# Kernel optimization log

Hardware: AMD Instinct MI355X
Metric: run time of the kernel (lower is better)

## Reference

```python
import jax, jax.numpy as jnp
import numpy as np

N_RES = 30000
N_ATOMS = 6
N_EDGES = 300000
HIDDEN = 128
N_GRAPHS = 32
CENTRAL_IDX = 1
EPS = 1e-6


def _normalize(x, axis=-1):
    # matches torch F.normalize (eps=1e-12 on the norm)
    return x / jnp.maximum(jnp.linalg.norm(x, axis=axis, keepdims=True), 1e-12)


def _rbf(D, D_min=0.0, D_max=20.0, num_rbf=16):
    mu = jnp.linspace(D_min, D_max, num_rbf)
    sigma = (D_max - D_min) / num_rbf
    return jnp.exp(-(((D[..., None] - mu) / sigma) ** 2))


def _quaternions(R):
    Rxx, Ryy, Rzz = R[:, 0, 0], R[:, 1, 1], R[:, 2, 2]
    mag = 0.5 * jnp.sqrt(jnp.abs(1.0 + jnp.stack([Rxx - Ryy - Rzz, -Rxx + Ryy - Rzz, -Rxx - Ryy + Rzz], -1)))
    signs = jnp.sign(jnp.stack([R[:, 2, 1] - R[:, 1, 2], R[:, 0, 2] - R[:, 2, 0], R[:, 1, 0] - R[:, 0, 1]], -1))
    xyz = signs * mag
    w = jnp.sqrt(jax.nn.relu(1.0 + Rxx + Ryy + Rzz))[:, None] / 2.0
    return _normalize(jnp.concatenate([xyz, w], -1))


def _layernorm(x, w, b, eps=1e-5):
    mu = x.mean(-1, keepdims=True)
    var = ((x - mu) ** 2).mean(-1, keepdims=True)
    return (x - mu) / jnp.sqrt(var + eps) * w + b


def _forward(coords, central_coords, node_W, node_b, node_ln_w, node_ln_b,
             edge_W, edge_b, edge_ln_w, edge_ln_b, batch, edge_index):
    n_res, n_atoms = coords.shape[:2]
    L = n_res * n_atoms
    src, tgt = edge_index[0], edge_index[1]

    # chain-boundary masks (replace torch's NaN-write + nan_to_num with masking to 0)
    boundary = jnp.concatenate([jnp.zeros(1, bool), batch[1:] != batch[:-1]])      # first res of new graph
    boundary_next = jnp.concatenate([boundary[1:], jnp.zeros(1, bool)])            # last res of a graph

    Xf = coords.reshape(-1, 3)
    ar = jnp.arange(L)
    col = jnp.arange(n_atoms)

    # ---- dihedral ----
    U = _normalize(Xf[1:] - Xf[:-1])
    c1 = _normalize(jnp.cross(U[:-2], U[1:-1]))
    c2 = _normalize(jnp.cross(U[1:-1], U[2:]))
    dih = jnp.arccos(jnp.clip((c1 * c2).sum(-1), -1.0 + EPS, 1.0 - EPS)) * jnp.sign((c2 * U[:-2]).sum(-1))
    dih = jnp.pad(dih, (1, 2)).reshape(n_res, n_atoms)
    d_mask = ((ar > 0) & (ar < L - 2)).reshape(n_res, n_atoms)
    d_mask = d_mask & ~(boundary[:, None] & (col == 0)[None])
    d_mask = d_mask & ~(boundary_next[:, None] & (col >= n_atoms - 2)[None])
    dih_feat = jnp.where(d_mask[..., None], jnp.stack([jnp.sin(dih), jnp.cos(dih)], -1), 0.0).reshape(n_res, -1)

    # ---- bond angle ----
    dX0 = _normalize(Xf[:-2] - Xf[1:-1])
    dX1 = _normalize(Xf[2:] - Xf[1:-1])
    cosang = (dX0 * dX1).sum(-1)
    sinang = jnp.sqrt(1.0 - cosang ** 2 + EPS)
    cosang = jnp.pad(cosang, (1, 1)).reshape(n_res, n_atoms)
    sinang = jnp.pad(sinang, (1, 1)).reshape(n_res, n_atoms)
    a_mask = ((ar > 0) & (ar < L - 1)).reshape(n_res, n_atoms)
    a_mask = a_mask & ~(boundary[:, None] & (col == 0)[None])
    a_mask = a_mask & ~(boundary_next[:, None] & (col == n_atoms - 1)[None])
    ang_feat = jnp.where(a_mask[..., None], jnp.stack([sinang, cosang], -1), 0.0).reshape(n_res, -1)

    # ---- local frame Q ----
    cX = central_coords
    du = _normalize(cX[1:] - cX[:-1])
    bvec = _normalize(du[:-1] - du[1:])
    nvec = _normalize(jnp.cross(du[:-1], du[1:]))
    Q = jnp.stack([bvec, nvec, jnp.cross(bvec, nvec)], -1)          # [n_res-2, 3, 3]
    Q = jnp.pad(Q, ((1, 1), (0, 0), (0, 0)))
    r = jnp.arange(n_res)
    q_valid = (r > 0) & (r < n_res - 1) & (~boundary) & (~boundary_next)
    Q = Q * q_valid[:, None, None]                                   # invalid frames -> 0 (== nan_to_num result)

    # ---- relative orientation quaternion per edge ----
    R = jnp.einsum('eki,ekj->eij', Q[tgt], Q[src])                   # tgt_Q^T @ src_Q
    orient = jnp.where((q_valid[src] & q_valid[tgt])[:, None], _quaternions(R), 0.0)

    # ---- inter distances / directions (edge) ----
    diff = coords[src][:, None, :, :] - coords[tgt][:, :, None, :]   # [E, n_atoms_t, n_atoms_s, 3]
    inter_D = jnp.sqrt((diff ** 2).sum(-1) + EPS)
    inter_dist = _rbf(inter_D).reshape(diff.shape[0], -1)            # [E, 576]
    inter_direct = jnp.einsum('eki,etsk->etsi', Q[tgt], _normalize(diff)).reshape(diff.shape[0], -1)  # [E, 108]

    # ---- intra distances / directions (node) ----
    keep = np.arange(n_atoms) != CENTRAL_IDX
    d_nc = coords[:, keep] - cX[:, None]                             # [n_res, 5, 3]
    intra_dist = jnp.log(jnp.sqrt((d_nc ** 2).sum(-1) + EPS))        # [n_res, 5]
    intra_direct = jnp.einsum('rki,rak->rai', Q, _normalize(d_nc)).reshape(n_res, -1)  # [n_res, 15]

    h_V = jnp.concatenate([dih_feat, ang_feat, intra_dist, intra_direct], -1)  # [n_res, 44]
    h_E = jnp.concatenate([orient, inter_dist, inter_direct], -1)              # [E, 688]
    h_V = _layernorm(h_V @ node_W + node_b, node_ln_w, node_ln_b)
    h_E = _layernorm(h_E @ edge_W + edge_b, edge_ln_w, edge_ln_b)
    return h_V, h_E


def setup_inputs() -> dict:
    key = jax.random.key(0)
    ks = jax.random.split(key, 8)
    coords = jax.random.normal(ks[0], (N_RES, N_ATOMS, 3), jnp.float32)
    central_coords = jax.random.normal(ks[1], (N_RES, 3), jnp.float32)
    batch = jnp.sort(jax.random.randint(ks[2], (N_RES,), 0, N_GRAPHS))
    edge_index = jax.random.randint(ks[3], (2, N_EDGES), 0, N_RES)
    node_W = jax.random.normal(ks[4], (44, HIDDEN), jnp.float32) / np.sqrt(44.0)
    edge_W = jax.random.normal(ks[5], (688, HIDDEN), jnp.float32) / np.sqrt(688.0)
    return {
        'coords': coords, 'central_coords': central_coords,
        'node_W': node_W, 'node_b': jnp.zeros((HIDDEN,), jnp.float32),
        'node_ln_w': jnp.ones((HIDDEN,), jnp.float32), 'node_ln_b': jnp.zeros((HIDDEN,), jnp.float32),
        'edge_W': edge_W, 'edge_b': jnp.zeros((HIDDEN,), jnp.float32),
        'edge_ln_w': jnp.ones((HIDDEN,), jnp.float32), 'edge_ln_b': jnp.zeros((HIDDEN,), jnp.float32),
        'batch': batch, 'edge_index': edge_index,
    }


def reference(coords, central_coords, node_W, node_b, node_ln_w, node_ln_b,
              edge_W, edge_b, edge_ln_w, edge_ln_b, batch, edge_index):
    return _forward(coords, central_coords, node_W, node_b, node_ln_w, node_ln_b,
                    edge_W, edge_b, edge_ln_w, edge_ln_b, batch, edge_index)
```

## Files before the change

### kernel.cpp

```cpp
#include <hip/hip_runtime.h>
#include <hip/hip_bf16.h>


#define N_RES   30000
#define N_ATOMS 6
#define LFLAT   (N_RES * N_ATOMS)
#define N_EDGES 300000
#define HID     128
#define NODE_IN 44
#define EDGE_IN 688
#define KSTEPS  43
#define EPSF    1e-6f
#define LN_EPS  1e-5f
#define MTILE   32

typedef unsigned short ushort_t;
typedef short short8 __attribute__((ext_vector_type(8)));
typedef float float16v __attribute__((ext_vector_type(16)));

static __device__ __forceinline__ unsigned short f2bf(float x) {
    __hip_bfloat16 h = __float2bfloat16(x);
    unsigned short u;
    __builtin_memcpy(&u, &h, 2);
    return u;
}

struct F3 { float x, y, z; };
static __device__ __forceinline__ F3 ld3(const float* p, long idx) {
    F3 r; r.x = p[idx*3+0]; r.y = p[idx*3+1]; r.z = p[idx*3+2]; return r;
}
static __device__ __forceinline__ F3 subv(F3 a, F3 b) { return {a.x-b.x, a.y-b.y, a.z-b.z}; }
static __device__ __forceinline__ float dotv(F3 a, F3 b) { return a.x*b.x + a.y*b.y + a.z*b.z; }
static __device__ __forceinline__ F3 crossv(F3 a, F3 b) {
    return {a.y*b.z - a.z*b.y, a.z*b.x - a.x*b.z, a.x*b.y - a.y*b.x};
}
static __device__ __forceinline__ F3 nrmv(F3 a) {
    float n = sqrtf(dotv(a, a));
    float inv = 1.f / fmaxf(n, 1e-12f);
    return {a.x*inv, a.y*inv, a.z*inv};
}
static __device__ __forceinline__ float sgn(float x) { return (x > 0.f) ? 1.f : ((x < 0.f) ? -1.f : 0.f); }

__global__ void k_packw(const float* __restrict__ W, unsigned short* __restrict__ Wp) {
    int s = blockIdx.x;
    int tid = threadIdx.x;
    int w = tid >> 6, lane = tid & 63;
    int ch = w * 32 + (lane & 31);
    int kh = lane >> 5;
    uint4 out;
    uint u[4];
    #pragma unroll
    for (int jp = 0; jp < 4; ++jp) {
        unsigned int lohi[2];
        #pragma unroll
        for (int b = 0; b < 2; ++b) {
            int jj = 2 * jp + b;
            int kn = 16 * s + kh * 8 + jj;
            int ko = (kn < 684) ? (kn + 4) : (kn - 684);
            lohi[b] = f2bf(W[(long)ko * HID + ch]);
        }
        u[jp] = lohi[0] | (lohi[1] << 16);
    }
    out.x = u[0]; out.y = u[1]; out.z = u[2]; out.w = u[3];
    *(uint4*)(Wp + ((size_t)(s * 4 + w) * 64 + lane) * 8) = out;
}

__global__ void k_frames(const float* __restrict__ central, const int* __restrict__ batch,
                         float* __restrict__ Qbuf, int* __restrict__ qval) {
    int r = blockIdx.x * 256 + threadIdx.x;
    if (r >= N_RES) return;
    bool bnd   = (r > 0)         && (batch[r]   != batch[r-1]);
    bool bndn  = (r < N_RES - 1) && (batch[r+1] != batch[r]);
    bool valid = (r > 0) && (r < N_RES - 1) && !bnd && !bndn;
    float Q[9] = {0,0,0,0,0,0,0,0,0};
    if (valid) {
        F3 cp = ld3(central, (long)r-1), cc = ld3(central, (long)r), cn = ld3(central, (long)r+1);
        F3 u0 = nrmv(subv(cc, cp));
        F3 u1 = nrmv(subv(cn, cc));
        F3 b  = nrmv(subv(u0, u1));
        F3 n  = nrmv(crossv(u0, u1));
        F3 c  = crossv(b, n);
        Q[0]=b.x; Q[1]=n.x; Q[2]=c.x;
        Q[3]=b.y; Q[4]=n.y; Q[5]=c.y;
        Q[6]=b.z; Q[7]=n.z; Q[8]=c.z;
    }
    #pragma unroll
    for (int k = 0; k < 9; k++) Qbuf[(size_t)r*9 + k] = Q[k];
    qval[r] = valid ? 1 : 0;
}

__global__ __launch_bounds__(HID) void k_node(
    const float* __restrict__ coords, const float* __restrict__ central,
    const float* __restrict__ node_W, const float* __restrict__ node_b,
    const float* __restrict__ lnw, const float* __restrict__ lnb,
    const int* __restrict__ batch, const float* __restrict__ Qbuf,
    float* __restrict__ out) {
    int r = blockIdx.x;
    int tid = threadIdx.x;
    __shared__ float feat[NODE_IN];
    __shared__ float red[4];

    if (tid < 6) {
        int c = tid;
        long j = (long)r * N_ATOMS + c;
        bool bnd  = (r > 0)         && (batch[r]   != batch[r-1]);
        bool bndn = (r < N_RES - 1) && (batch[r+1] != batch[r]);
        float sd = 0.f, cd = 0.f;
        bool dm = (j > 0) && (j < LFLAT - 2) && !(bnd && c == 0) && !(bndn && c >= N_ATOMS - 2);
        if (dm) {
            F3 x0 = ld3(coords, j-1), x1 = ld3(coords, j), x2 = ld3(coords, j+1), x3 = ld3(coords, j+2);
            F3 u1 = nrmv(subv(x1, x0)), u2 = nrmv(subv(x2, x1)), u3 = nrmv(subv(x3, x2));
            F3 c1 = nrmv(crossv(u1, u2)), c2 = nrmv(crossv(u2, u3));
            float cc = fminf(fmaxf(dotv(c1, c2), -1.f + EPSF), 1.f - EPSF);
            float D  = acosf(cc) * sgn(dotv(c2, u1));
            sd = sinf(D); cd = cosf(D);
        }
        feat[2*c] = sd; feat[2*c+1] = cd;
        float sa = 0.f, ca = 0.f;
        bool am = (j > 0) && (j < LFLAT - 1) && !(bnd && c == 0) && !(bndn && c == N_ATOMS - 1);
        if (am) {
            F3 x0 = ld3(coords, j-1), x1 = ld3(coords, j), x2 = ld3(coords, j+1);
            F3 d0 = nrmv(subv(x0, x1)), d1 = nrmv(subv(x2, x1));
            float cv = dotv(d0, d1);
            sa = sqrtf(1.f - cv*cv + EPSF);
            ca = cv;
        }
        feat[12 + 2*c] = sa; feat[12 + 2*c + 1] = ca;
    } else if (tid < 11) {
        int a = tid - 6;
        int atom = (a == 0) ? 0 : (a + 1);
        F3 x  = ld3(coords, (long)r * N_ATOMS + atom);
        F3 cx = ld3(central, (long)r);
        F3 d  = subv(x, cx);
        float d2 = dotv(d, d);
        feat[24 + a] = 0.5f * logf(d2 + EPSF);
        float inv = 1.f / fmaxf(sqrtf(d2), 1e-12f);
        float nx = d.x*inv, ny = d.y*inv, nz = d.z*inv;
        const float* Q = Qbuf + (size_t)r * 9;
        #pragma unroll
        for (int i = 0; i < 3; i++)
            feat[29 + a*3 + i] = Q[0+i]*nx + Q[3+i]*ny + Q[6+i]*nz;
    }
    __syncthreads();

    float acc = node_b[tid];
    #pragma unroll
    for (int i = 0; i < NODE_IN; i++)
        acc += feat[i] * node_W[(long)i * HID + tid];

    float s = acc;
    #pragma unroll
    for (int m = 1; m < 64; m <<= 1) s += __shfl_xor(s, m, 64);
    int wv = tid >> 6;
    if ((tid & 63) == 0) red[wv] = s;
    __syncthreads();
    float mu = (red[0] + red[1]) * (1.f / HID);
    float dv = acc - mu;
    float q = dv * dv;
    #pragma unroll
    for (int m = 1; m < 64; m <<= 1) q += __shfl_xor(q, m, 64);
    if ((tid & 63) == 0) red[2 + wv] = q;
    __syncthreads();
    float var = (red[2] + red[3]) * (1.f / HID);
    float y = dv * rsqrtf(var + LN_EPS) * lnw[tid] + lnb[tid];
    out[(size_t)r * HID + tid] = y;
}

__global__ __launch_bounds__(256) void k_edge(
    const float* __restrict__ coords, const int* __restrict__ eidx,
    const unsigned short* __restrict__ Wpack, const float* __restrict__ edge_b,
    const float* __restrict__ lnw, const float* __restrict__ lnb,
    const float* __restrict__ Qbuf, const int* __restrict__ qval,
    float* __restrict__ outE) {
    __shared__ __align__(16) unsigned char smemA[KSTEPS * 64 * 8 * 2];
    __shared__ float qtS[MTILE][9];
    __shared__ int sS[MTILE], tS[MTILE];

    unsigned short* Ast = (unsigned short*)smemA;
    int tid = threadIdx.x;
    int lane = tid & 63;
    int w = tid >> 6;
    int e0 = blockIdx.x * MTILE;

    if (tid < MTILE) {
        int ge = e0 + tid;
        int s = eidx[ge];
        int t = eidx[N_EDGES + ge];
        sS[tid] = s; tS[tid] = t;
        float Qs[9], Qt[9];
        #pragma unroll
        for (int k = 0; k < 9; k++) {
            Qs[k] = Qbuf[(size_t)s*9 + k];
            Qt[k] = Qbuf[(size_t)t*9 + k];
            qtS[tid][k] = Qt[k];
        }
        float R[9];
        #pragma unroll
        for (int i = 0; i < 3; i++)
            #pragma unroll
            for (int jj = 0; jj < 3; jj++)
                R[i*3+jj] = Qt[0+i]*Qs[0+jj] + Qt[3+i]*Qs[3+jj] + Qt[6+i]*Qs[6+jj];
        float m0 = 0.5f * sqrtf(fabsf(1.f + R[0] - R[4] - R[8]));
        float m1 = 0.5f * sqrtf(fabsf(1.f - R[0] + R[4] - R[8]));
        float m2 = 0.5f * sqrtf(fabsf(1.f - R[0] - R[4] + R[8]));
        float xq = sgn(R[7] - R[5]) * m0;
        float yq = sgn(R[2] - R[6]) * m1;
        float zq = sgn(R[3] - R[1]) * m2;
        float wq = 0.5f * sqrtf(fmaxf(1.f + R[0] + R[4] + R[8], 0.f));
        float nq = sqrtf(xq*xq + yq*yq + zq*zq + wq*wq);
        float inv = 1.f / fmaxf(nq, 1e-12f);
        float vm = (qval[s] && qval[t]) ? 1.f : 0.f;
        unsigned int p0 = f2bf(xq * inv * vm) | ((unsigned int)f2bf(yq * inv * vm) << 16);
        unsigned int p1 = f2bf(zq * inv * vm) | ((unsigned int)f2bf(wq * inv * vm) << 16);
        uint2 pk; pk.x = p0; pk.y = p1;
        *(uint2*)(Ast + ((42 * 64 + 32 + tid) * 8 + 4)) = pk;
    }
    __syncthreads();

    for (int task = tid; task < 36 * MTILE; task += 256) {
        int e = task & (MTILE - 1);
        int pair = task >> 5;
        int ta = pair / 6, sa = pair - ta * 6;
        int s = sS[e], t = tS[e];
        F3 cs = ld3(coords, (long)s * N_ATOMS + sa);
        F3 ct = ld3(coords, (long)t * N_ATOMS + ta);
        float dx = cs.x - ct.x, dy = cs.y - ct.y, dz = cs.z - ct.z;
        float d2 = dx*dx + dy*dy + dz*dz;
        float D = sqrtf(d2 + EPSF);
        unsigned int u[8];
        #pragma unroll
        for (int i = 0; i < 8; i++) {
            float z0 = (D - (float)(2*i)   * (4.f/3.f)) * 0.8f;
            float z1 = (D - (float)(2*i+1) * (4.f/3.f)) * 0.8f;
            u[i] = f2bf(__expf(-z0*z0)) | ((unsigned int)f2bf(__expf(-z1*z1)) << 16);
        }
        uint4 lo; lo.x = u[0]; lo.y = u[1]; lo.z = u[2]; lo.w = u[3];
        uint4 hi; hi.x = u[4]; hi.y = u[5]; hi.z = u[6]; hi.w = u[7];
        *(uint4*)(Ast + (pair * 64 + e) * 8)      = lo;
        *(uint4*)(Ast + (pair * 64 + 32 + e) * 8) = hi;
        float inv = 1.f / fmaxf(sqrtf(d2), 1e-12f);
        float nx = dx*inv, ny = dy*inv, nz = dz*inv;
        #pragma unroll
        for (int i = 0; i < 3; i++) {
            float v = qtS[e][0+i]*nx + qtS[e][3+i]*ny + qtS[e][6+i]*nz;
            int kn = 576 + pair * 3 + i;
            int s2 = kn >> 4, r2 = kn & 15;
            Ast[((s2 * 64) + (r2 >> 3) * 32 + e) * 8 + (r2 & 7)] = f2bf(v);
        }
    }
    __syncthreads();

    float16v acc;
    #pragma unroll
    for (int i = 0; i < 16; i++) acc[i] = 0.f;
    const short8* Ap = (const short8*)smemA;
    const short8* Bp = (const short8*)Wpack;
    for (int s = 0; s < KSTEPS; ++s) {
        short8 a = Ap[s * 64 + lane];
        short8 b = Bp[(s * 4 + w) * 64 + lane];
        acc = __builtin_amdgcn_mfma_f32_32x32x16_bf16(a, b, acc, 0, 0, 0);
    }

    __syncthreads();
    float* C_s = (float*)smemA;
    int col = lane & 31;
    #pragma unroll
    for (int r = 0; r < 16; ++r) {
        int row = (r & 3) + 8 * (r >> 2) + 4 * (lane >> 5);
        C_s[row * 132 + w * 32 + col] = acc[r];
    }
    __syncthreads();

    int e = tid >> 3;
    int p = tid & 7;
    const float* Crow = C_s + e * 132 + p * 16;
    float x[16];
    float sum = 0.f;
    #pragma unroll
    for (int j = 0; j < 16; ++j) {
        x[j] = Crow[j] + edge_b[p * 16 + j];
        sum += x[j];
    }
    #pragma unroll
    for (int m = 1; m < 8; m <<= 1) sum += __shfl_xor(sum, m, 64);
    float mu = sum * (1.f / HID);
    float vs = 0.f;
    #pragma unroll
    for (int j = 0; j < 16; ++j) { float d = x[j] - mu; vs += d * d; }
    #pragma unroll
    for (int m = 1; m < 8; m <<= 1) vs += __shfl_xor(vs, m, 64);
    float is = rsqrtf(vs * (1.f / HID) + LN_EPS);
    float* op = outE + (size_t)(e0 + e) * HID + p * 16;
    #pragma unroll
    for (int j = 0; j < 16; ++j) {
        int ch = p * 16 + j;
        op[j] = (x[j] - mu) * is * lnw[ch] + lnb[ch];
    }
}

extern "C" void kernel_launch(void* const* d_in, const int* in_sizes, int n_in,
                              void* d_out, int out_size, void* d_ws, size_t ws_size,
                              hipStream_t stream) {
    (void)in_sizes; (void)n_in; (void)out_size; (void)ws_size;
    const float* coords  = (const float*)d_in[0];
    const float* central = (const float*)d_in[1];
    const float* node_W  = (const float*)d_in[2];
    const float* node_b  = (const float*)d_in[3];
    const float* node_lw = (const float*)d_in[4];
    const float* node_lb = (const float*)d_in[5];
    const float* edge_W  = (const float*)d_in[6];
    const float* edge_b  = (const float*)d_in[7];
    const float* edge_lw = (const float*)d_in[8];
    const float* edge_lb = (const float*)d_in[9];
    const int*   batch   = (const int*)d_in[10];
    const int*   eidx    = (const int*)d_in[11];

    unsigned short* Wpack = (unsigned short*)d_ws;
    float* Qbuf = (float*)((char*)d_ws + (size_t)EDGE_IN * HID * 2);
    int*   qval = (int*)(Qbuf + (size_t)N_RES * 9);

    float* outV = (float*)d_out;
    float* outE = outV + (size_t)N_RES * HID;

    hipLaunchKernelGGL(k_packw,  dim3(KSTEPS),            dim3(256), 0, stream, edge_W, Wpack);
    hipLaunchKernelGGL(k_frames, dim3((N_RES + 255)/256), dim3(256), 0, stream, central, batch, Qbuf, qval);
    hipLaunchKernelGGL(k_node,   dim3(N_RES),             dim3(HID), 0, stream,
                       coords, central, node_W, node_b, node_lw, node_lb, batch, Qbuf, outV);
    hipLaunchKernelGGL(k_edge,   dim3(N_EDGES / MTILE),   dim3(256), 0, stream,
                       coords, eidx, Wpack, edge_b, edge_lw, edge_lb, Qbuf, qval, outE);
}
```

Before: 368.7 us.

## Split edge A-tile into two K phases, stage coords in LDS, use rsqrt math

The edge kernel now keeps only 32 K-steps of the A tile in LDS instead of 43. It runs the MFMA loop over the first 32, then reuses the buffer for the remaining RBF pairs, direction features and quaternion before finishing the last 11 K-steps. Coordinates for source and target residues are staged cooperatively in shared memory, and launch bounds request 4 blocks per CU. Dihedral sin/cos drops acos/sin/cos for an algebraic form, and sqrt/divide pairs become rsqrt, trading extra syncs and some recomputation for lower LDS use and higher occupancy.

```diff
diff --git a/kernel.cpp b/kernel.cpp
--- a/kernel.cpp
+++ b/kernel.cpp
@@ -10,6 +10,7 @@
 #define NODE_IN 44
 #define EDGE_IN 688
 #define KSTEPS  43
+#define KS_A    32
 #define EPSF    1e-6f
 #define LN_EPS  1e-5f
 #define MTILE   32
@@ -35,8 +36,7 @@
     return {a.y*b.z - a.z*b.y, a.z*b.x - a.x*b.z, a.x*b.y - a.y*b.x};
 }
 static __device__ __forceinline__ F3 nrmv(F3 a) {
-    float n = sqrtf(dotv(a, a));
-    float inv = 1.f / fmaxf(n, 1e-12f);
+    float inv = rsqrtf(fmaxf(dotv(a, a), 1e-24f));
     return {a.x*inv, a.y*inv, a.z*inv};
 }
 static __device__ __forceinline__ float sgn(float x) { return (x > 0.f) ? 1.f : ((x < 0.f) ? -1.f : 0.f); }
@@ -112,8 +112,9 @@
             F3 u1 = nrmv(subv(x1, x0)), u2 = nrmv(subv(x2, x1)), u3 = nrmv(subv(x3, x2));
             F3 c1 = nrmv(crossv(u1, u2)), c2 = nrmv(crossv(u2, u3));
             float cc = fminf(fmaxf(dotv(c1, c2), -1.f + EPSF), 1.f - EPSF);
-            float D  = acosf(cc) * sgn(dotv(c2, u1));
-            sd = sinf(D); cd = cosf(D);
+            float s  = sgn(dotv(c2, u1));
+            sd = s * sqrtf(fmaxf(1.f - cc*cc, 0.f));
+            cd = (s != 0.f) ? cc : 1.f;
         }
         feat[2*c] = sd; feat[2*c+1] = cd;
         float sa = 0.f, ca = 0.f;
@@ -122,7 +123,8 @@
             F3 x0 = ld3(coords, j-1), x1 = ld3(coords, j), x2 = ld3(coords, j+1);
             F3 d0 = nrmv(subv(x0, x1)), d1 = nrmv(subv(x2, x1));
             float cv = dotv(d0, d1);
-            sa = sqrtf(1.f - cv*cv + EPSF);
+            float t = 1.f - cv*cv + EPSF;
+            sa = t * rsqrtf(t);
             ca = cv;
         }
         feat[12 + 2*c] = sa; feat[12 + 2*c + 1] = ca;
@@ -133,8 +135,8 @@
         F3 cx = ld3(central, (long)r);
         F3 d  = subv(x, cx);
         float d2 = dotv(d, d);
-        feat[24 + a] = 0.5f * logf(d2 + EPSF);
-        float inv = 1.f / fmaxf(sqrtf(d2), 1e-12f);
+        feat[24 + a] = 0.5f * __logf(d2 + EPSF);
+        float inv = rsqrtf(fmaxf(d2, 1e-24f));
         float nx = d.x*inv, ny = d.y*inv, nz = d.z*inv;
         const float* Q = Qbuf + (size_t)r * 9;
         #pragma unroll
@@ -166,13 +168,14 @@
     out[(size_t)r * HID + tid] = y;
 }
 
-__global__ __launch_bounds__(256) void k_edge(
+__global__ __launch_bounds__(256, 4) void k_edge(
     const float* __restrict__ coords, const int* __restrict__ eidx,
     const unsigned short* __restrict__ Wpack, const float* __restrict__ edge_b,
     const float* __restrict__ lnw, const float* __restrict__ lnb,
     const float* __restrict__ Qbuf, const int* __restrict__ qval,
     float* __restrict__ outE) {
-    __shared__ __align__(16) unsigned char smemA[KSTEPS * 64 * 8 * 2];
+    __shared__ __align__(16) unsigned char smemA[KS_A * 64 * 8 * 2];
+    __shared__ float cS[64][18];
     __shared__ float qtS[MTILE][9];
     __shared__ int sS[MTILE], tS[MTILE];
 
@@ -183,10 +186,26 @@
     int e0 = blockIdx.x * MTILE;
 
     if (tid < MTILE) {
-        int ge = e0 + tid;
-        int s = eidx[ge];
-        int t = eidx[N_EDGES + ge];
-        sS[tid] = s; tS[tid] = t;
+        sS[tid] = eidx[e0 + tid];
+        tS[tid] = eidx[N_EDGES + e0 + tid];
+    }
+    __syncthreads();
+
+    #pragma unroll
+    for (int it = 0; it < 5; ++it) {
+        int idx = tid + it * 256;
+        if (idx < 64 * 18) {
+            int slot = idx / 18;
+            int rem  = idx - slot * 18;
+            int res  = (slot < 32) ? sS[slot] : tS[slot - 32];
+            cS[slot][rem] = coords[(size_t)res * 18 + rem];
+        }
+    }
+
+    uint2 qpk;
+    if (tid < MTILE) {
+        int s = sS[tid];
+        int t = tS[tid];
         float Qs[9], Qt[9];
         #pragma unroll
         for (int k = 0; k < 9; k++) {
@@ -207,46 +226,45 @@
         float yq = sgn(R[2] - R[6]) * m1;
         float zq = sgn(R[3] - R[1]) * m2;
         float wq = 0.5f * sqrtf(fmaxf(1.f + R[0] + R[4] + R[8], 0.f));
-        float nq = sqrtf(xq*xq + yq*yq + zq*zq + wq*wq);
-        float inv = 1.f / fmaxf(nq, 1e-12f);
+        float nq2 = xq*xq + yq*yq + zq*zq + wq*wq;
+        float inv = rsqrtf(fmaxf(nq2, 1e-24f));
         float vm = (qval[s] && qval[t]) ? 1.f : 0.f;
-        unsigned int p0 = f2bf(xq * inv * vm) | ((unsigned int)f2bf(yq * inv * vm) << 16);
-        unsigned int p1 = f2bf(zq * inv * vm) | ((unsigned int)f2bf(wq * inv * vm) << 16);
-        uint2 pk; pk.x = p0; pk.y = p1;
-        *(uint2*)(Ast + ((42 * 64 + 32 + tid) * 8 + 4)) = pk;
-    }
-    __syncthreads();
-
-    for (int task = tid; task < 36 * MTILE; task += 256) {
-        int e = task & (MTILE - 1);
-        int pair = task >> 5;
+        qpk.x = f2bf(xq * inv * vm) | ((unsigned int)f2bf(yq * inv * vm) << 16);
+        qpk.y = f2bf(zq * inv * vm) | ((unsigned int)f2bf(wq * inv * vm) << 16);
+    }
+    __syncthreads();
+
+    int e  = tid & 31;
+    int p0 = tid >> 5;
+
+    float vdir[4][3];
+    #pragma unroll
+    for (int it = 0; it < 4; ++it) {
+        int pair = p0 + 8 * it;
         int ta = pair / 6, sa = pair - ta * 6;
-        int s = sS[e], t = tS[e];
-        F3 cs = ld3(coords, (long)s * N_ATOMS + sa);
-        F3 ct = ld3(coords, (long)t * N_ATOMS + ta);
-        float dx = cs.x - ct.x, dy = cs.y - ct.y, dz = cs.z - ct.z;
+        float dx = cS[e][sa*3+0] - cS[32+e][ta*3+0];
+        float dy = cS[e][sa*3+1] - cS[32+e][ta*3+1];
+        float dz = cS[e][sa*3+2] - cS[32+e][ta*3+2];
         float d2 = dx*dx + dy*dy + dz*dz;
-        float D = sqrtf(d2 + EPSF);
+        float t  = d2 + EPSF;
+        float D  = t * rsqrtf(t);
+        float a8 = D * 0.8f;
         unsigned int u[8];
         #pragma unroll
         for (int i = 0; i < 8; i++) {
-            float z0 = (D - (float)(2*i)   * (4.f/3.f)) * 0.8f;
-            float z1 = (D - (float)(2*i+1) * (4.f/3.f)) * 0.8f;
-            u[i] = f2bf(__expf(-z0*z0)) | ((unsigned int)f2bf(__expf(-z1*z1)) << 16);
+            float z0 = a8 - (float)(2*i)     * 1.06666672f;
+            float z1 = a8 - (float)(2*i + 1) * 1.06666672f;
+            u[i] = f2bf(__expf(-(z0*z0))) | ((unsigned int)f2bf(__expf(-(z1*z1))) << 16);
         }
         uint4 lo; lo.x = u[0]; lo.y = u[1]; lo.z = u[2]; lo.w = u[3];
         uint4 hi; hi.x = u[4]; hi.y = u[5]; hi.z = u[6]; hi.w = u[7];
         *(uint4*)(Ast + (pair * 64 + e) * 8)      = lo;
         *(uint4*)(Ast + (pair * 64 + 32 + e) * 8) = hi;
-        float inv = 1.f / fmaxf(sqrtf(d2), 1e-12f);
+        float inv = rsqrtf(fmaxf(d2, 1e-24f));
         float nx = dx*inv, ny = dy*inv, nz = dz*inv;
         #pragma unroll
-        for (int i = 0; i < 3; i++) {
-            float v = qtS[e][0+i]*nx + qtS[e][3+i]*ny + qtS[e][6+i]*nz;
-            int kn = 576 + pair * 3 + i;
-            int s2 = kn >> 4, r2 = kn & 15;
-            Ast[((s2 * 64) + (r2 >> 3) * 32 + e) * 8 + (r2 & 7)] = f2bf(v);
-        }
+        for (int i = 0; i < 3; i++)
+            vdir[it][i] = qtS[e][0+i]*nx + qtS[e][3+i]*ny + qtS[e][6+i]*nz;
     }
     __syncthreads();
 
@@ -255,11 +273,65 @@
     for (int i = 0; i < 16; i++) acc[i] = 0.f;
     const short8* Ap = (const short8*)smemA;
     const short8* Bp = (const short8*)Wpack;
-    for (int s = 0; s < KSTEPS; ++s) {
+    for (int s = 0; s < KS_A; ++s) {
         short8 a = Ap[s * 64 + lane];
         short8 b = Bp[(s * 4 + w) * 64 + lane];
         acc = __builtin_amdgcn_mfma_f32_32x32x16_bf16(a, b, acc, 0, 0, 0);
     }
+    __syncthreads();
+
+    if (tid < 128) {
+        int e2 = tid & 31;
+        int pair = 32 + (tid >> 5);
+        int ta = pair / 6, sa = pair - ta * 6;
+        float dx = cS[e2][sa*3+0] - cS[32+e2][ta*3+0];
+        float dy = cS[e2][sa*3+1] - cS[32+e2][ta*3+1];
+        float dz = cS[e2][sa*3+2] - cS[32+e2][ta*3+2];
+        float d2 = dx*dx + dy*dy + dz*dz;
+        float t  = d2 + EPSF;
+        float D  = t * rsqrtf(t);
+        float a8 = D * 0.8f;
+        unsigned int u[8];
+        #pragma unroll
+        for (int i = 0; i < 8; i++) {
+            float z0 = a8 - (float)(2*i)     * 1.06666672f;
+            float z1 = a8 - (float)(2*i + 1) * 1.06666672f;
+            u[i] = f2bf(__expf(-(z0*z0))) | ((unsigned int)f2bf(__expf(-(z1*z1))) << 16);
+        }
+        uint4 lo; lo.x = u[0]; lo.y = u[1]; lo.z = u[2]; lo.w = u[3];
+        uint4 hi; hi.x = u[4]; hi.y = u[5]; hi.z = u[6]; hi.w = u[7];
+        int lks = pair - 32;
+        *(uint4*)(Ast + (lks * 64 + e2) * 8)      = lo;
+        *(uint4*)(Ast + (lks * 64 + 32 + e2) * 8) = hi;
+        float inv = rsqrtf(fmaxf(d2, 1e-24f));
+        float nx = dx*inv, ny = dy*inv, nz = dz*inv;
+        #pragma unroll
+        for (int i = 0; i < 3; i++) {
+            float v = qtS[e2][0+i]*nx + qtS[e2][3+i]*ny + qtS[e2][6+i]*nz;
+            int kn = 576 + pair * 3 + i;
+            int s2 = kn >> 4, r2 = kn & 15;
+            Ast[(((s2 - 32) * 64) + (r2 >> 3) * 32 + e2) * 8 + (r2 & 7)] = f2bf(v);
+        }
+    }
+    #pragma unroll
+    for (int it = 0; it < 4; ++it) {
+        int pair = p0 + 8 * it;
+        #pragma unroll
+        for (int i = 0; i < 3; i++) {
+            int kn = 576 + pair * 3 + i;
+            int s2 = kn >> 4, r2 = kn & 15;
+            Ast[(((s2 - 32) * 64) + (r2 >> 3) * 32 + e) * 8 + (r2 & 7)] = f2bf(vdir[it][i]);
+        }
+    }
+    if (tid < MTILE)
+        *(uint2*)(Ast + ((10 * 64 + 32 + tid) * 8 + 4)) = qpk;
+    __syncthreads();
+
+    for (int s = KS_A; s < KSTEPS; ++s) {
+        short8 a = Ap[(s - KS_A) * 64 + lane];
+        short8 b = Bp[(s * 4 + w) * 64 + lane];
+        acc = __builtin_amdgcn_mfma_f32_32x32x16_bf16(a, b, acc, 0, 0, 0);
+    }
 
     __syncthreads();
     float* C_s = (float*)smemA;
@@ -271,9 +343,9 @@
     }
     __syncthreads();
 
-    int e = tid >> 3;
-    int p = tid & 7;
-    const float* Crow = C_s + e * 132 + p * 16;
+    int ee = tid >> 3;
+    int p  = tid & 7;
+    const float* Crow = C_s + ee * 132 + p * 16;
     float x[16];
     float sum = 0.f;
     #pragma unroll
@@ -290,7 +362,7 @@
     #pragma unroll
     for (int m = 1; m < 8; m <<= 1) vs += __shfl_xor(vs, m, 64);
     float is = rsqrtf(vs * (1.f / HID) + LN_EPS);
-    float* op = outE + (size_t)(e0 + e) * HID + p * 16;
+    float* op = outE + (size_t)(e0 + ee) * HID + p * 16;
     #pragma unroll
     for (int j = 0; j < 16; ++j) {
         int ch = p * 16 + j;
```

After: 339.3 us. -8.0%, faster.
